# Performance work log

Measured on AMD Instinct MI355X. Metric: run time of the kernel, lower is better.

Reference implementation:

```python
import jax, jax.numpy as jnp
import numpy as np

LEAK = 0.9  # leaky-integrator rate of the ESN cell


def setup_inputs() -> dict:
    key = jax.random.key(0)
    ks = jax.random.split(key, 7)
    S, B, I, R = 512, 64, 256, 2048
    sc_in0 = 1.0 / np.sqrt(I)
    sc_h = 0.9 / np.sqrt(R)  # ~spectral-radius style scaling
    sc_in1 = 1.0 / np.sqrt(R)
    return {
        "x": jax.random.normal(ks[0], (S, B, I), jnp.float32),
        "W_in0": jax.random.normal(ks[1], (R, I), jnp.float32) * sc_in0,
        "W_hh0": jax.random.normal(ks[2], (R, R), jnp.float32) * sc_h,
        "b0": jax.random.normal(ks[3], (R,), jnp.float32) * 0.1,
        "W_in1": jax.random.normal(ks[4], (R, R), jnp.float32) * sc_in1,
        "W_hh1": jax.random.normal(ks[5], (R, R), jnp.float32) * sc_h,
        "b1": jax.random.normal(ks[6], (R,), jnp.float32) * 0.1,
    }


def _esn_layer(x_seq, W_in, W_hh, b):
    # x_seq: (S, B, D_in); returns (S, B, R), (B, R)
    B = x_seq.shape[1]
    R = W_hh.shape[0]
    h0 = jnp.zeros((B, R), x_seq.dtype)
    # Precompute input projection for all timesteps in one big GEMM.
    xin = jnp.einsum('sbd,rd->sbr', x_seq, W_in) + b

    def step(h, xin_t):
        h_new = (1.0 - LEAK) * h + LEAK * jnp.tanh(xin_t + h @ W_hh.T)
        return h_new, h_new

    h_n, ys = jax.lax.scan(step, h0, xin)
    return ys, h_n


def reference(x, W_in0, W_hh0, b0, W_in1, W_hh1, b1):
    y0, h0n = _esn_layer(x, W_in0, W_hh0, b0)
    y1, h1n = _esn_layer(y0, W_in1, W_hh1, b1)
    h_n = jnp.stack([h0n, h1n])  # (num_layers, B, R)
    return y1, h_n
```

## Files before the change

### kernel.cpp

```cpp
#include <hip/hip_runtime.h>

typedef _Float16 half8 __attribute__((ext_vector_type(8)));
typedef float floatx4 __attribute__((ext_vector_type(4)));

#define S_LEN 512
#define NB 64
#define NI 256
#define NR 2048
#define LEAK 0.9f

#define NBLK 128
#define TPB 512
#define LBLK 64
#define NBNR ((size_t)NB * NR)

#define OFF_BAR ((size_t)0)
#define OFF_H0  ((size_t)4096)
#define OFF_H1  (OFF_H0 + 2 * NBNR * 2)
#define OFF_XE  (OFF_H1 + 2 * NBNR * 2)

__device__ __forceinline__ half8 cvt8(const float* s) {
    float4 p = *(const float4*)s, q = *(const float4*)(s + 4);
    half8 v;
    v[0] = (_Float16)p.x; v[1] = (_Float16)p.y; v[2] = (_Float16)p.z; v[3] = (_Float16)p.w;
    v[4] = (_Float16)q.x; v[5] = (_Float16)q.y; v[6] = (_Float16)q.z; v[7] = (_Float16)q.w;
    return v;
}

__global__ void xprep_kernel(const float* __restrict__ x, _Float16* __restrict__ xe) {
    const int t = blockIdx.x;
    #pragma unroll
    for (int it = 0; it < 4; ++it) {
        const int u = it * 8 + (threadIdx.x >> 6);
        const int l = threadIdx.x & 63;
        const int b = (u >> 3) * 16 + (l & 15);
        const int i0 = (u & 7) * 32 + (l >> 4) * 8;
        half8 v = cvt8(x + ((size_t)t * NB + b) * NI + i0);
        *(half8*)(xe + (size_t)t * NB * NI + (size_t)u * 512 + (size_t)l * 8) = v;
    }
}

__device__ __forceinline__ void gbar(unsigned* bar) {
    __syncthreads();
    if (threadIdx.x == 0) {
        __threadfence();
        unsigned* cnt  = bar + (blockIdx.x & 7) * 32;
        unsigned* root = bar + 256;
        unsigned* gen  = bar + 272;
        unsigned g = __hip_atomic_load(gen, __ATOMIC_RELAXED, __HIP_MEMORY_SCOPE_AGENT);
        bool last = false;
        if (__hip_atomic_fetch_add(cnt, 1u, __ATOMIC_ACQ_REL, __HIP_MEMORY_SCOPE_AGENT) == (NBLK / 8 - 1)) {
            __hip_atomic_store(cnt, 0u, __ATOMIC_RELAXED, __HIP_MEMORY_SCOPE_AGENT);
            if (__hip_atomic_fetch_add(root, 1u, __ATOMIC_ACQ_REL, __HIP_MEMORY_SCOPE_AGENT) == 7u) {
                __hip_atomic_store(root, 0u, __ATOMIC_RELAXED, __HIP_MEMORY_SCOPE_AGENT);
                __hip_atomic_store(gen, g + 1u, __ATOMIC_RELEASE, __HIP_MEMORY_SCOPE_AGENT);
                last = true;
            }
        }
        if (!last)
            while (__hip_atomic_load(gen, __ATOMIC_RELAXED, __HIP_MEMORY_SCOPE_AGENT) == g)
                __builtin_amdgcn_s_sleep(1);
        __threadfence();
    }
    __syncthreads();
}

template <int CH, int KU, int ROLE>
__device__ __forceinline__ void esn_layer_run(
    const float* __restrict__ bias_v,
    const float* __restrict__ Whh, const float* __restrict__ Win,
    const char* __restrict__ xe,
    char* __restrict__ hp,
    const char* __restrict__ h0p,
    float* __restrict__ out,
    unsigned* __restrict__ bar,
    float* __restrict__ rsc, int r0)
{
    const int tid = threadIdx.x;
    const int l = tid & 63, w = tid >> 6, l15 = l & 15, g = l >> 4;

    half8 bwA[CH], bwB[CH];
    #pragma unroll
    for (int j = 0; j < CH; ++j) {
        const float* s0; int rs;
        if (j < 8) { s0 = Whh + (size_t)(r0 + l15) * NR + (w * 8 + j) * 32 + g * 8; rs = NR; }
        else if (ROLE == 0) { s0 = Win + (size_t)(r0 + l15) * KU + w * 32 + g * 8; rs = KU; }
        else { s0 = Win + (size_t)(r0 + l15) * KU + (w * 8 + j - 8) * 32 + g * 8; rs = KU; }
        bwA[j] = cvt8(s0);
        bwB[j] = cvt8(s0 + (size_t)16 * rs);
    }

    const int fg_o = w & 1, bt_o = w >> 1;
    const int ncol = r0 + fg_o * 16 + l15;
    const int bj0 = bt_o * 16 + g * 4;
    const float bias = bias_v[ncol];
    const int cu = ncol >> 5, gg = (ncol >> 3) & 3, ee = ncol & 7;
    float hs[4] = {0.f, 0.f, 0.f, 0.f};
    float* hn_base = out + (size_t)S_LEN * NBNR + (size_t)ROLE * NBNR;

    for (int s = 0; s < S_LEN + 1; ++s) {
        const int t = (ROLE == 0) ? s : s - 1;
        const bool active = (ROLE == 0) ? (s < S_LEN) : (s >= 1);
        if (active) {
            const char* hu = hp + (size_t)(t & 1) * (NBNR * 2);
            const char* uu = (ROLE == 0) ? xe + (size_t)t * NB * NI * 2
                                         : h0p + (size_t)((t + 1) & 1) * (NBNR * 2);

            floatx4 acc[2][4];
            #pragma unroll
            for (int fg = 0; fg < 2; ++fg)
                #pragma unroll
                for (int bt = 0; bt < 4; ++bt)
                    acc[fg][bt] = (floatx4){0.f, 0.f, 0.f, 0.f};

            #pragma unroll
            for (int bt = 0; bt < 4; ++bt) {
                half8 abuf[CH];
                #pragma unroll
                for (int j = 0; j < CH; ++j) {
                    const char* src; size_t unit;
                    if (j < 8)          { src = hu; unit = (size_t)(bt * 64 + w * 8 + j); }
                    else if (ROLE == 0) { src = uu; unit = (size_t)(bt * 8 + w); }
                    else                { src = uu; unit = (size_t)(bt * 64 + w * 8 + j - 8); }
                    abuf[j] = *(const half8*)(src + unit * 1024 + (size_t)l * 16);
                }
                #pragma unroll
                for (int j = 0; j < CH; ++j) {
                    acc[0][bt] = __builtin_amdgcn_mfma_f32_16x16x32_f16(abuf[j], bwA[j], acc[0][bt], 0, 0, 0);
                    acc[1][bt] = __builtin_amdgcn_mfma_f32_16x16x32_f16(abuf[j], bwB[j], acc[1][bt], 0, 0, 0);
                }
            }

            #pragma unroll
            for (int fg = 0; fg < 2; ++fg)
                #pragma unroll
                for (int bt = 0; bt < 4; ++bt)
                    *(floatx4*)(rsc + (size_t)((w * 8 + fg * 4 + bt) * 64 + l) * 4) = acc[fg][bt];
            __syncthreads();

            floatx4 r = {0.f, 0.f, 0.f, 0.f};
            #pragma unroll
            for (int v = 0; v < 8; ++v)
                r += *(const floatx4*)(rsc + (size_t)((v * 8 + fg_o * 4 + bt_o) * 64 + l) * 4);

            char* hw = hp + (size_t)((t + 1) & 1) * (NBNR * 2);
            #pragma unroll
            for (int j = 0; j < 4; ++j) {
                float hn = (1.0f - LEAK) * hs[j] + LEAK * tanhf(r[j] + bias);
                hs[j] = hn;
                const int bj = bj0 + j;
                size_t byte = (size_t)((bj >> 4) * 64 + cu) * 1024
                            + (size_t)((gg * 16 + (bj & 15)) * 8 + ee) * 2;
                *(_Float16*)(hw + byte) = (_Float16)hn;
                if (ROLE == 1)
                    __builtin_nontemporal_store(hn, out + (size_t)t * NBNR + (size_t)bj * NR + ncol);
                if (t == S_LEN - 1)
                    __builtin_nontemporal_store(hn, hn_base + (size_t)bj * NR + ncol);
            }
        }
        if (s < S_LEN) gbar(bar);
    }
}

__global__ void __launch_bounds__(TPB, 1) esn_kernel(
    const float* __restrict__ b0v, const float* __restrict__ b1v,
    const float* __restrict__ Whh0, const float* __restrict__ Win0,
    const float* __restrict__ Whh1, const float* __restrict__ Win1,
    const char* __restrict__ xe,
    char* __restrict__ h0p, char* __restrict__ h1p,
    unsigned* __restrict__ bar, float* __restrict__ out)
{
    __shared__ __align__(16) float rsc[64 * 64 * 4];
    const int bid = blockIdx.x;
    if (bid < LBLK)
        esn_layer_run<9, NI, 0>(b0v, Whh0, Win0, xe, h0p, nullptr,
                                out, bar, rsc, bid * 32);
    else
        esn_layer_run<16, NR, 1>(b1v, Whh1, Win1, nullptr, h1p, h0p,
                                 out, bar, rsc, (bid - LBLK) * 32);
}

extern "C" void kernel_launch(void* const* d_in, const int* in_sizes, int n_in,
                              void* d_out, int out_size, void* d_ws, size_t ws_size,
                              hipStream_t stream) {
    const float* x    = (const float*)d_in[0];
    const float* Win0 = (const float*)d_in[1];
    const float* Whh0 = (const float*)d_in[2];
    const float* b0   = (const float*)d_in[3];
    const float* Win1 = (const float*)d_in[4];
    const float* Whh1 = (const float*)d_in[5];
    const float* b1   = (const float*)d_in[6];

    char* ws = (char*)d_ws;
    char* xe  = ws + OFF_XE;
    char* h0p = ws + OFF_H0;
    char* h1p = ws + OFF_H1;
    unsigned* bar = (unsigned*)(ws + OFF_BAR);
    float* out = (float*)d_out;

    hipMemsetAsync(ws, 0, OFF_XE, stream);

    xprep_kernel<<<dim3(S_LEN), dim3(512), 0, stream>>>(x, (_Float16*)xe);

    void* args[] = { (void*)&b0, (void*)&b1, (void*)&Whh0, (void*)&Win0,
                     (void*)&Whh1, (void*)&Win1, (void*)&xe, (void*)&h0p,
                     (void*)&h1p, (void*)&bar, (void*)&out };
    hipError_t e = hipLaunchCooperativeKernel((void*)esn_kernel, dim3(NBLK), dim3(TPB),
                                              args, 0, stream);
    if (e != hipSuccess) {
        esn_kernel<<<dim3(NBLK), dim3(TPB), 0, stream>>>(
            b0, b1, Whh0, Win0, Whh1, Win1, xe, h0p, h1p, bar, out);
    }
}
```

Baseline: 8.902 ms.

## Split each ESN block's batch in half across 256 cooperative blocks with lighter barrier

```diff
diff --git a/kernel.cpp b/kernel.cpp
--- a/kernel.cpp
+++ b/kernel.cpp
@@ -9,9 +9,8 @@
 #define NR 2048
 #define LEAK 0.9f
 
-#define NBLK 128
+#define NBLK 256
 #define TPB 512
-#define LBLK 64
 #define NBNR ((size_t)NB * NR)
 
 #define OFF_BAR ((size_t)0)
@@ -40,16 +39,21 @@
     }
 }
 
+__device__ __forceinline__ void stH(_Float16* p, _Float16 v) {
+    unsigned short b;
+    __builtin_memcpy(&b, &v, 2);
+    __hip_atomic_store((unsigned short*)p, b, __ATOMIC_RELAXED, __HIP_MEMORY_SCOPE_AGENT);
+}
+
 __device__ __forceinline__ void gbar(unsigned* bar) {
     __syncthreads();
     if (threadIdx.x == 0) {
-        __threadfence();
         unsigned* cnt  = bar + (blockIdx.x & 7) * 32;
         unsigned* root = bar + 256;
         unsigned* gen  = bar + 272;
         unsigned g = __hip_atomic_load(gen, __ATOMIC_RELAXED, __HIP_MEMORY_SCOPE_AGENT);
         bool last = false;
-        if (__hip_atomic_fetch_add(cnt, 1u, __ATOMIC_ACQ_REL, __HIP_MEMORY_SCOPE_AGENT) == (NBLK / 8 - 1)) {
+        if (__hip_atomic_fetch_add(cnt, 1u, __ATOMIC_RELAXED, __HIP_MEMORY_SCOPE_AGENT) == (NBLK / 8 - 1)) {
             __hip_atomic_store(cnt, 0u, __ATOMIC_RELAXED, __HIP_MEMORY_SCOPE_AGENT);
             if (__hip_atomic_fetch_add(root, 1u, __ATOMIC_ACQ_REL, __HIP_MEMORY_SCOPE_AGENT) == 7u) {
                 __hip_atomic_store(root, 0u, __ATOMIC_RELAXED, __HIP_MEMORY_SCOPE_AGENT);
@@ -59,10 +63,10 @@
         }
         if (!last)
             while (__hip_atomic_load(gen, __ATOMIC_RELAXED, __HIP_MEMORY_SCOPE_AGENT) == g)
-                __builtin_amdgcn_s_sleep(1);
-        __threadfence();
+                __builtin_amdgcn_s_sleep(2);
     }
     __syncthreads();
+    __builtin_amdgcn_fence(__ATOMIC_ACQUIRE, "agent");
 }
 
 template <int CH, int KU, int ROLE>
@@ -74,7 +78,7 @@
     const char* __restrict__ h0p,
     float* __restrict__ out,
     unsigned* __restrict__ bar,
-    float* __restrict__ rsc, int r0)
+    float* __restrict__ rsc, int r0, int bhalf)
 {
     const int tid = threadIdx.x;
     const int l = tid & 63, w = tid >> 6, l15 = l & 15, g = l >> 4;
@@ -88,12 +92,14 @@
         else { s0 = Win + (size_t)(r0 + l15) * KU + (w * 8 + j - 8) * 32 + g * 8; rs = KU; }
         bwA[j] = cvt8(s0);
         bwB[j] = cvt8(s0 + (size_t)16 * rs);
-    }
-
-    const int fg_o = w & 1, bt_o = w >> 1;
+        asm volatile("" : "+v"(bwA[j]));
+        asm volatile("" : "+v"(bwB[j]));
+    }
+
+    const int fg_o = w & 1, bt_o = (w >> 1) & 1;
+    const bool owner = (w < 4);
     const int ncol = r0 + fg_o * 16 + l15;
-    const int bj0 = bt_o * 16 + g * 4;
-    const float bias = bias_v[ncol];
+    const float bias = owner ? bias_v[ncol] : 0.f;
     const int cu = ncol >> 5, gg = (ncol >> 3) & 3, ee = ncol & 7;
     float hs[4] = {0.f, 0.f, 0.f, 0.f};
     float* hn_base = out + (size_t)S_LEN * NBNR + (size_t)ROLE * NBNR;
@@ -106,22 +112,23 @@
             const char* uu = (ROLE == 0) ? xe + (size_t)t * NB * NI * 2
                                          : h0p + (size_t)((t + 1) & 1) * (NBNR * 2);
 
-            floatx4 acc[2][4];
+            floatx4 acc[2][2];
             #pragma unroll
             for (int fg = 0; fg < 2; ++fg)
                 #pragma unroll
-                for (int bt = 0; bt < 4; ++bt)
+                for (int bt = 0; bt < 2; ++bt)
                     acc[fg][bt] = (floatx4){0.f, 0.f, 0.f, 0.f};
 
             #pragma unroll
-            for (int bt = 0; bt < 4; ++bt) {
+            for (int bt = 0; bt < 2; ++bt) {
+                const int bt_g = bhalf * 2 + bt;
                 half8 abuf[CH];
                 #pragma unroll
                 for (int j = 0; j < CH; ++j) {
                     const char* src; size_t unit;
-                    if (j < 8)          { src = hu; unit = (size_t)(bt * 64 + w * 8 + j); }
-                    else if (ROLE == 0) { src = uu; unit = (size_t)(bt * 8 + w); }
-                    else                { src = uu; unit = (size_t)(bt * 64 + w * 8 + j - 8); }
+                    if (j < 8)          { src = hu; unit = (size_t)(bt_g * 64 + w * 8 + j); }
+                    else if (ROLE == 0) { src = uu; unit = (size_t)(bt_g * 8 + w); }
+                    else                { src = uu; unit = (size_t)(bt_g * 64 + w * 8 + j - 8); }
                     abuf[j] = *(const half8*)(src + unit * 1024 + (size_t)l * 16);
                 }
                 #pragma unroll
@@ -134,35 +141,37 @@
             #pragma unroll
             for (int fg = 0; fg < 2; ++fg)
                 #pragma unroll
-                for (int bt = 0; bt < 4; ++bt)
-                    *(floatx4*)(rsc + (size_t)((w * 8 + fg * 4 + bt) * 64 + l) * 4) = acc[fg][bt];
+                for (int bt = 0; bt < 2; ++bt)
+                    *(floatx4*)(rsc + (size_t)((w * 4 + bt * 2 + fg) * 64 + l) * 4) = acc[fg][bt];
             __syncthreads();
 
-            floatx4 r = {0.f, 0.f, 0.f, 0.f};
-            #pragma unroll
-            for (int v = 0; v < 8; ++v)
-                r += *(const floatx4*)(rsc + (size_t)((v * 8 + fg_o * 4 + bt_o) * 64 + l) * 4);
-
-            char* hw = hp + (size_t)((t + 1) & 1) * (NBNR * 2);
-            #pragma unroll
-            for (int j = 0; j < 4; ++j) {
-                float hn = (1.0f - LEAK) * hs[j] + LEAK * tanhf(r[j] + bias);
-                hs[j] = hn;
-                const int bj = bj0 + j;
-                size_t byte = (size_t)((bj >> 4) * 64 + cu) * 1024
-                            + (size_t)((gg * 16 + (bj & 15)) * 8 + ee) * 2;
-                *(_Float16*)(hw + byte) = (_Float16)hn;
-                if (ROLE == 1)
-                    __builtin_nontemporal_store(hn, out + (size_t)t * NBNR + (size_t)bj * NR + ncol);
-                if (t == S_LEN - 1)
-                    __builtin_nontemporal_store(hn, hn_base + (size_t)bj * NR + ncol);
+            if (owner) {
+                floatx4 r = {0.f, 0.f, 0.f, 0.f};
+                #pragma unroll
+                for (int v = 0; v < 8; ++v)
+                    r += *(const floatx4*)(rsc + (size_t)((v * 4 + w) * 64 + l) * 4);
+
+                char* hw = hp + (size_t)((t + 1) & 1) * (NBNR * 2);
+                #pragma unroll
+                for (int j = 0; j < 4; ++j) {
+                    float hn = (1.0f - LEAK) * hs[j] + LEAK * tanhf(r[j] + bias);
+                    hs[j] = hn;
+                    const int bj = bhalf * 32 + bt_o * 16 + g * 4 + j;
+                    size_t byte = (size_t)((bj >> 4) * 64 + cu) * 1024
+                                + (size_t)((gg * 16 + (bj & 15)) * 8 + ee) * 2;
+                    stH((_Float16*)(hw + byte), (_Float16)hn);
+                    if (ROLE == 1)
+                        __builtin_nontemporal_store(hn, out + (size_t)t * NBNR + (size_t)bj * NR + ncol);
+                    if (t == S_LEN - 1)
+                        __builtin_nontemporal_store(hn, hn_base + (size_t)bj * NR + ncol);
+                }
             }
         }
         if (s < S_LEN) gbar(bar);
     }
 }
 
-__global__ void __launch_bounds__(TPB, 1) esn_kernel(
+__global__ void __launch_bounds__(TPB, 2) esn_kernel(
     const float* __restrict__ b0v, const float* __restrict__ b1v,
     const float* __restrict__ Whh0, const float* __restrict__ Win0,
     const float* __restrict__ Whh1, const float* __restrict__ Win1,
@@ -170,14 +179,17 @@
     char* __restrict__ h0p, char* __restrict__ h1p,
     unsigned* __restrict__ bar, float* __restrict__ out)
 {
-    __shared__ __align__(16) float rsc[64 * 64 * 4];
+    __shared__ __align__(16) float rsc[32 * 64 * 4];
     const int bid = blockIdx.x;
-    if (bid < LBLK)
+    const int sub = bid & 127;
+    const int r0 = (sub >> 1) * 32;
+    const int bhalf = sub & 1;
+    if (bid < 128)
         esn_layer_run<9, NI, 0>(b0v, Whh0, Win0, xe, h0p, nullptr,
-                                out, bar, rsc, bid * 32);
+                                out, bar, rsc, r0, bhalf);
     else
         esn_layer_run<16, NR, 1>(b1v, Whh1, Win1, nullptr, h1p, h0p,
-                                 out, bar, rsc, (bid - LBLK) * 32);
+                                 out, bar, rsc, r0, bhalf);
 }
 
 extern "C" void kernel_launch(void* const* d_in, const int* in_sizes, int n_in,
@@ -198,7 +210,7 @@
     unsigned* bar = (unsigned*)(ws + OFF_BAR);
     float* out = (float*)d_out;
 
-    hipMemsetAsync(ws, 0, OFF_XE, stream);
+    (void)hipMemsetAsync(ws, 0, OFF_XE, stream);
 
     xprep_kernel<<<dim3(S_LEN), dim3(512), 0, stream>>>(x, (_Float16*)xe);
 
```

After: 10.98 ms. +23.3%, slower.

## Stream pre-converted fp16 weights each step instead of holding them in registers

Applied to the files above, without the earlier changes.

```diff
diff --git a/kernel.cpp b/kernel.cpp
--- a/kernel.cpp
+++ b/kernel.cpp
@@ -14,10 +14,19 @@
 #define LBLK 64
 #define NBNR ((size_t)NB * NR)
 
+#define CHT0 72
+#define CHT1 128
+
 #define OFF_BAR ((size_t)0)
 #define OFF_H0  ((size_t)4096)
 #define OFF_H1  (OFF_H0 + 2 * NBNR * 2)
 #define OFF_XE  (OFF_H1 + 2 * NBNR * 2)
+#define SZ_XE   ((size_t)S_LEN * NB * NI * 2)
+#define OFF_W0  (OFF_XE + SZ_XE)
+#define SZ_W0   ((size_t)128 * CHT0 * 1024)
+#define OFF_W1  (OFF_W0 + SZ_W0)
+#define SZ_W1   ((size_t)128 * CHT1 * 1024)
+#define WS_NEED (OFF_W1 + SZ_W1)
 
 __device__ __forceinline__ half8 cvt8(const float* s) {
     float4 p = *(const float4*)s, q = *(const float4*)(s + 4);
@@ -38,6 +47,22 @@
         half8 v = cvt8(x + ((size_t)t * NB + b) * NI + i0);
         *(half8*)(xe + (size_t)t * NB * NI + (size_t)u * 512 + (size_t)l * 8) = v;
     }
+}
+
+__global__ void wprep_kernel(const float* __restrict__ Whh0, const float* __restrict__ Win0,
+                             const float* __restrict__ Whh1, const float* __restrict__ Win1,
+                             _Float16* __restrict__ w0f, _Float16* __restrict__ w1f) {
+    int unit = blockIdx.x * 4 + (threadIdx.x >> 6);
+    const int l = threadIdx.x & 63;
+    const float* Whh; const float* Win; _Float16* dst; int CHT, KU;
+    if (unit < 128 * CHT0) { Whh = Whh0; Win = Win0; dst = w0f; CHT = CHT0; KU = NI; }
+    else { unit -= 128 * CHT0; Whh = Whh1; Win = Win1; dst = w1f; CHT = CHT1; KU = NR; }
+    const int fg = unit / CHT, ch = unit - fg * CHT;
+    const int feat = fg * 16 + (l & 15);
+    const int k = ch * 32 + (l >> 4) * 8;
+    const float* src = (k < NR) ? Whh + (size_t)feat * NR + k
+                                : Win + (size_t)feat * KU + (k - NR);
+    *(half8*)(dst + ((size_t)unit << 9) + (size_t)l * 8) = cvt8(src);
 }
 
 __device__ __forceinline__ void gbar(unsigned* bar) {
@@ -65,30 +90,27 @@
     __syncthreads();
 }
 
-template <int CH, int KU, int ROLE>
+__device__ __forceinline__ void stage8(half8* d, const char* src, int unitbase, int l) {
+    #pragma unroll
+    for (int jj = 0; jj < 8; ++jj)
+        d[jj] = *(const half8*)(src + ((size_t)(unitbase + jj) << 10) + (size_t)l * 16);
+}
+
+template <int ROLE, bool WF16>
 __device__ __forceinline__ void esn_layer_run(
     const float* __restrict__ bias_v,
-    const float* __restrict__ Whh, const float* __restrict__ Win,
+    const float* Whh, const float* Win,
+    const _Float16* __restrict__ wf,
     const char* __restrict__ xe,
-    char* __restrict__ hp,
-    const char* __restrict__ h0p,
+    char* hp, const char* h0p,
     float* __restrict__ out,
     unsigned* __restrict__ bar,
     float* __restrict__ rsc, int r0)
 {
     const int tid = threadIdx.x;
     const int l = tid & 63, w = tid >> 6, l15 = l & 15, g = l >> 4;
-
-    half8 bwA[CH], bwB[CH];
-    #pragma unroll
-    for (int j = 0; j < CH; ++j) {
-        const float* s0; int rs;
-        if (j < 8) { s0 = Whh + (size_t)(r0 + l15) * NR + (w * 8 + j) * 32 + g * 8; rs = NR; }
-        else if (ROLE == 0) { s0 = Win + (size_t)(r0 + l15) * KU + w * 32 + g * 8; rs = KU; }
-        else { s0 = Win + (size_t)(r0 + l15) * KU + (w * 8 + j - 8) * 32 + g * 8; rs = KU; }
-        bwA[j] = cvt8(s0);
-        bwB[j] = cvt8(s0 + (size_t)16 * rs);
-    }
+    constexpr int CHT = ROLE ? CHT1 : CHT0;
+    const int fg0 = r0 >> 4;
 
     const int fg_o = w & 1, bt_o = w >> 1;
     const int ncol = r0 + fg_o * 16 + l15;
@@ -113,21 +135,76 @@
                 for (int bt = 0; bt < 4; ++bt)
                     acc[fg][bt] = (floatx4){0.f, 0.f, 0.f, 0.f};
 
+            half8 wA[8], wB[8], ab[2][8];
+
+            if (WF16) {
+                const _Float16* p0 = wf + (((size_t)fg0 * CHT + w * 8) << 9) + (size_t)l * 8;
+                const _Float16* p1 = wf + (((size_t)(fg0 + 1) * CHT + w * 8) << 9) + (size_t)l * 8;
+                #pragma unroll
+                for (int jj = 0; jj < 8; ++jj) {
+                    wA[jj] = *(const half8*)(p0 + ((size_t)jj << 9));
+                    wB[jj] = *(const half8*)(p1 + ((size_t)jj << 9));
+                }
+            } else {
+                #pragma unroll
+                for (int jj = 0; jj < 8; ++jj) {
+                    wA[jj] = cvt8(Whh + (size_t)(r0 + l15) * NR + (w * 8 + jj) * 32 + g * 8);
+                    wB[jj] = cvt8(Whh + (size_t)(r0 + 16 + l15) * NR + (w * 8 + jj) * 32 + g * 8);
+                }
+            }
+            stage8(ab[0], hu, w * 8, l);
             #pragma unroll
             for (int bt = 0; bt < 4; ++bt) {
-                half8 abuf[CH];
-                #pragma unroll
-                for (int j = 0; j < CH; ++j) {
-                    const char* src; size_t unit;
-                    if (j < 8)          { src = hu; unit = (size_t)(bt * 64 + w * 8 + j); }
-                    else if (ROLE == 0) { src = uu; unit = (size_t)(bt * 8 + w); }
-                    else                { src = uu; unit = (size_t)(bt * 64 + w * 8 + j - 8); }
-                    abuf[j] = *(const half8*)(src + unit * 1024 + (size_t)l * 16);
-                }
-                #pragma unroll
-                for (int j = 0; j < CH; ++j) {
-                    acc[0][bt] = __builtin_amdgcn_mfma_f32_16x16x32_f16(abuf[j], bwA[j], acc[0][bt], 0, 0, 0);
-                    acc[1][bt] = __builtin_amdgcn_mfma_f32_16x16x32_f16(abuf[j], bwB[j], acc[1][bt], 0, 0, 0);
+                if (bt < 3) stage8(ab[(bt + 1) & 1], hu, (bt + 1) * 64 + w * 8, l);
+                #pragma unroll
+                for (int jj = 0; jj < 8; ++jj) {
+                    acc[0][bt] = __builtin_amdgcn_mfma_f32_16x16x32_f16(ab[bt & 1][jj], wA[jj], acc[0][bt], 0, 0, 0);
+                    acc[1][bt] = __builtin_amdgcn_mfma_f32_16x16x32_f16(ab[bt & 1][jj], wB[jj], acc[1][bt], 0, 0, 0);
+                }
+            }
+
+            if (ROLE == 1) {
+                if (WF16) {
+                    const _Float16* p0 = wf + (((size_t)fg0 * CHT + 64 + w * 8) << 9) + (size_t)l * 8;
+                    const _Float16* p1 = wf + (((size_t)(fg0 + 1) * CHT + 64 + w * 8) << 9) + (size_t)l * 8;
+                    #pragma unroll
+                    for (int jj = 0; jj < 8; ++jj) {
+                        wA[jj] = *(const half8*)(p0 + ((size_t)jj << 9));
+                        wB[jj] = *(const half8*)(p1 + ((size_t)jj << 9));
+                    }
+                } else {
+                    #pragma unroll
+                    for (int jj = 0; jj < 8; ++jj) {
+                        wA[jj] = cvt8(Win + (size_t)(r0 + l15) * NR + (w * 8 + jj) * 32 + g * 8);
+                        wB[jj] = cvt8(Win + (size_t)(r0 + 16 + l15) * NR + (w * 8 + jj) * 32 + g * 8);
+                    }
+                }
+                stage8(ab[0], uu, w * 8, l);
+                #pragma unroll
+                for (int bt = 0; bt < 4; ++bt) {
+                    if (bt < 3) stage8(ab[(bt + 1) & 1], uu, (bt + 1) * 64 + w * 8, l);
+                    #pragma unroll
+                    for (int jj = 0; jj < 8; ++jj) {
+                        acc[0][bt] = __builtin_amdgcn_mfma_f32_16x16x32_f16(ab[bt & 1][jj], wA[jj], acc[0][bt], 0, 0, 0);
+                        acc[1][bt] = __builtin_amdgcn_mfma_f32_16x16x32_f16(ab[bt & 1][jj], wB[jj], acc[1][bt], 0, 0, 0);
+                    }
+                }
+            } else {
+                half8 wiA, wiB, ai[4];
+                if (WF16) {
+                    wiA = *(const half8*)(wf + (((size_t)fg0 * CHT + 64 + w) << 9) + (size_t)l * 8);
+                    wiB = *(const half8*)(wf + (((size_t)(fg0 + 1) * CHT + 64 + w) << 9) + (size_t)l * 8);
+                } else {
+                    wiA = cvt8(Win + (size_t)(r0 + l15) * NI + w * 32 + g * 8);
+                    wiB = cvt8(Win + (size_t)(r0 + 16 + l15) * NI + w * 32 + g * 8);
+                }
+                #pragma unroll
+                for (int bt = 0; bt < 4; ++bt)
+                    ai[bt] = *(const half8*)(uu + ((size_t)(bt * 8 + w) << 10) + (size_t)l * 16);
+                #pragma unroll
+                for (int bt = 0; bt < 4; ++bt) {
+                    acc[0][bt] = __builtin_amdgcn_mfma_f32_16x16x32_f16(ai[bt], wiA, acc[0][bt], 0, 0, 0);
+                    acc[1][bt] = __builtin_amdgcn_mfma_f32_16x16x32_f16(ai[bt], wiB, acc[1][bt], 0, 0, 0);
                 }
             }
 
@@ -162,22 +239,24 @@
     }
 }
 
+template <bool WF16>
 __global__ void __launch_bounds__(TPB, 1) esn_kernel(
     const float* __restrict__ b0v, const float* __restrict__ b1v,
-    const float* __restrict__ Whh0, const float* __restrict__ Win0,
-    const float* __restrict__ Whh1, const float* __restrict__ Win1,
+    const float* Whh0, const float* Win0,
+    const float* Whh1, const float* Win1,
+    const _Float16* __restrict__ w0f, const _Float16* __restrict__ w1f,
     const char* __restrict__ xe,
-    char* __restrict__ h0p, char* __restrict__ h1p,
+    char* h0p, char* h1p,
     unsigned* __restrict__ bar, float* __restrict__ out)
 {
     __shared__ __align__(16) float rsc[64 * 64 * 4];
     const int bid = blockIdx.x;
     if (bid < LBLK)
-        esn_layer_run<9, NI, 0>(b0v, Whh0, Win0, xe, h0p, nullptr,
-                                out, bar, rsc, bid * 32);
+        esn_layer_run<0, WF16>(b0v, Whh0, Win0, w0f, xe, h0p, nullptr,
+                               out, bar, rsc, bid * 32);
     else
-        esn_layer_run<16, NR, 1>(b1v, Whh1, Win1, nullptr, h1p, h0p,
-                                 out, bar, rsc, (bid - LBLK) * 32);
+        esn_layer_run<1, WF16>(b1v, Whh1, Win1, w1f, nullptr, h1p, h0p,
+                               out, bar, rsc, (bid - LBLK) * 32);
 }
 
 extern "C" void kernel_launch(void* const* d_in, const int* in_sizes, int n_in,
@@ -196,19 +275,30 @@
     char* h0p = ws + OFF_H0;
     char* h1p = ws + OFF_H1;
     unsigned* bar = (unsigned*)(ws + OFF_BAR);
+    _Float16* w0f = (_Float16*)(ws + OFF_W0);
+    _Float16* w1f = (_Float16*)(ws + OFF_W1);
     float* out = (float*)d_out;
 
-    hipMemsetAsync(ws, 0, OFF_XE, stream);
-
+    const bool wf16 = (ws_size >= WS_NEED);
+
+    (void)hipMemsetAsync(ws, 0, OFF_XE, stream);
     xprep_kernel<<<dim3(S_LEN), dim3(512), 0, stream>>>(x, (_Float16*)xe);
+    if (wf16)
+        wprep_kernel<<<dim3((128 * (CHT0 + CHT1)) / 4), dim3(256), 0, stream>>>(
+            Whh0, Win0, Whh1, Win1, w0f, w1f);
 
     void* args[] = { (void*)&b0, (void*)&b1, (void*)&Whh0, (void*)&Win0,
-                     (void*)&Whh1, (void*)&Win1, (void*)&xe, (void*)&h0p,
-                     (void*)&h1p, (void*)&bar, (void*)&out };
-    hipError_t e = hipLaunchCooperativeKernel((void*)esn_kernel, dim3(NBLK), dim3(TPB),
+                     (void*)&Whh1, (void*)&Win1, (void*)&w0f, (void*)&w1f,
+                     (void*)&xe, (void*)&h0p, (void*)&h1p, (void*)&bar, (void*)&out };
+    void* fn = wf16 ? (void*)esn_kernel<true> : (void*)esn_kernel<false>;
+    hipError_t e = hipLaunchCooperativeKernel(fn, dim3(NBLK), dim3(TPB),
                                               args, 0, stream);
     if (e != hipSuccess) {
-        esn_kernel<<<dim3(NBLK), dim3(TPB), 0, stream>>>(
-            b0, b1, Whh0, Win0, Whh1, Win1, xe, h0p, h1p, bar, out);
+        if (wf16)
+            esn_kernel<true><<<dim3(NBLK), dim3(TPB), 0, stream>>>(
+                b0, b1, Whh0, Win0, Whh1, Win1, w0f, w1f, xe, h0p, h1p, bar, out);
+        else
+            esn_kernel<false><<<dim3(NBLK), dim3(TPB), 0, stream>>>(
+                b0, b1, Whh0, Win0, Whh1, Win1, w0f, w1f, xe, h0p, h1p, bar, out);
     }
 }
```

Result: slower. 9.593 ms (+7.8%).

## Double threads per block and split K reduction across 16 waves

Applied to the files above, without the earlier changes.

```diff
diff --git a/kernel.cpp b/kernel.cpp
--- a/kernel.cpp
+++ b/kernel.cpp
@@ -10,7 +10,7 @@
 #define LEAK 0.9f
 
 #define NBLK 128
-#define TPB 512
+#define TPB 1024
 #define LBLK 64
 #define NBNR ((size_t)NB * NR)
 
@@ -65,7 +65,7 @@
     __syncthreads();
 }
 
-template <int CH, int KU, int ROLE>
+template <int ROLE>
 __device__ __forceinline__ void esn_layer_run(
     const float* __restrict__ bias_v,
     const float* __restrict__ Whh, const float* __restrict__ Win,
@@ -78,22 +78,32 @@
 {
     const int tid = threadIdx.x;
     const int l = tid & 63, w = tid >> 6, l15 = l & 15, g = l >> 4;
-
-    half8 bwA[CH], bwB[CH];
+    constexpr int KU = ROLE ? NR : NI;
+
+    half8 wrA[4], wrB[4];
     #pragma unroll
-    for (int j = 0; j < CH; ++j) {
-        const float* s0; int rs;
-        if (j < 8) { s0 = Whh + (size_t)(r0 + l15) * NR + (w * 8 + j) * 32 + g * 8; rs = NR; }
-        else if (ROLE == 0) { s0 = Win + (size_t)(r0 + l15) * KU + w * 32 + g * 8; rs = KU; }
-        else { s0 = Win + (size_t)(r0 + l15) * KU + (w * 8 + j - 8) * 32 + g * 8; rs = KU; }
-        bwA[j] = cvt8(s0);
-        bwB[j] = cvt8(s0 + (size_t)16 * rs);
+    for (int j = 0; j < 4; ++j) {
+        const float* s = Whh + (size_t)(r0 + l15) * NR + (w * 4 + j) * 32 + g * 8;
+        wrA[j] = cvt8(s);
+        wrB[j] = cvt8(s + (size_t)16 * NR);
+    }
+    const int chi = (ROLE == 1) ? 4 : ((w >= 8) ? 1 : 0);
+    const int ci0 = (ROLE == 1) ? w * 4 : (w - 8);
+    half8 wiA[4], wiB[4];
+    #pragma unroll
+    for (int j = 0; j < 4; ++j) {
+        if (j < chi) {
+            const float* s = Win + (size_t)(r0 + l15) * KU + (ci0 + j) * 32 + g * 8;
+            wiA[j] = cvt8(s);
+            wiB[j] = cvt8(s + (size_t)16 * KU);
+        }
     }
 
     const int fg_o = w & 1, bt_o = w >> 1;
+    const bool owner = (w < 8);
     const int ncol = r0 + fg_o * 16 + l15;
     const int bj0 = bt_o * 16 + g * 4;
-    const float bias = bias_v[ncol];
+    const float bias = owner ? bias_v[ncol] : 0.f;
     const int cu = ncol >> 5, gg = (ncol >> 3) & 3, ee = ncol & 7;
     float hs[4] = {0.f, 0.f, 0.f, 0.f};
     float* hn_base = out + (size_t)S_LEN * NBNR + (size_t)ROLE * NBNR;
@@ -115,19 +125,30 @@
 
             #pragma unroll
             for (int bt = 0; bt < 4; ++bt) {
-                half8 abuf[CH];
-                #pragma unroll
-                for (int j = 0; j < CH; ++j) {
-                    const char* src; size_t unit;
-                    if (j < 8)          { src = hu; unit = (size_t)(bt * 64 + w * 8 + j); }
-                    else if (ROLE == 0) { src = uu; unit = (size_t)(bt * 8 + w); }
-                    else                { src = uu; unit = (size_t)(bt * 64 + w * 8 + j - 8); }
-                    abuf[j] = *(const half8*)(src + unit * 1024 + (size_t)l * 16);
-                }
-                #pragma unroll
-                for (int j = 0; j < CH; ++j) {
-                    acc[0][bt] = __builtin_amdgcn_mfma_f32_16x16x32_f16(abuf[j], bwA[j], acc[0][bt], 0, 0, 0);
-                    acc[1][bt] = __builtin_amdgcn_mfma_f32_16x16x32_f16(abuf[j], bwB[j], acc[1][bt], 0, 0, 0);
+                half8 ar[4];
+                #pragma unroll
+                for (int j = 0; j < 4; ++j)
+                    ar[j] = *(const half8*)(hu + ((size_t)(bt * 64 + w * 4 + j) << 10) + (size_t)l * 16);
+                #pragma unroll
+                for (int j = 0; j < 4; ++j) {
+                    acc[0][bt] = __builtin_amdgcn_mfma_f32_16x16x32_f16(ar[j], wrA[j], acc[0][bt], 0, 0, 0);
+                    acc[1][bt] = __builtin_amdgcn_mfma_f32_16x16x32_f16(ar[j], wrB[j], acc[1][bt], 0, 0, 0);
+                }
+                half8 av[4];
+                #pragma unroll
+                for (int j = 0; j < 4; ++j) {
+                    if (j < chi) {
+                        const size_t unit = (ROLE == 1) ? (size_t)(bt * 64 + ci0 + j)
+                                                        : (size_t)(bt * 8 + ci0);
+                        av[j] = *(const half8*)(uu + (unit << 10) + (size_t)l * 16);
+                    }
+                }
+                #pragma unroll
+                for (int j = 0; j < 4; ++j) {
+                    if (j < chi) {
+                        acc[0][bt] = __builtin_amdgcn_mfma_f32_16x16x32_f16(av[j], wiA[j], acc[0][bt], 0, 0, 0);
+                        acc[1][bt] = __builtin_amdgcn_mfma_f32_16x16x32_f16(av[j], wiB[j], acc[1][bt], 0, 0, 0);
+                    }
                 }
             }
 
@@ -138,24 +159,26 @@
                     *(floatx4*)(rsc + (size_t)((w * 8 + fg * 4 + bt) * 64 + l) * 4) = acc[fg][bt];
             __syncthreads();
 
-            floatx4 r = {0.f, 0.f, 0.f, 0.f};
-            #pragma unroll
-            for (int v = 0; v < 8; ++v)
-                r += *(const floatx4*)(rsc + (size_t)((v * 8 + fg_o * 4 + bt_o) * 64 + l) * 4);
-
-            char* hw = hp + (size_t)((t + 1) & 1) * (NBNR * 2);
-            #pragma unroll
-            for (int j = 0; j < 4; ++j) {
-                float hn = (1.0f - LEAK) * hs[j] + LEAK * tanhf(r[j] + bias);
-                hs[j] = hn;
-                const int bj = bj0 + j;
-                size_t byte = (size_t)((bj >> 4) * 64 + cu) * 1024
-                            + (size_t)((gg * 16 + (bj & 15)) * 8 + ee) * 2;
-                *(_Float16*)(hw + byte) = (_Float16)hn;
-                if (ROLE == 1)
-                    __builtin_nontemporal_store(hn, out + (size_t)t * NBNR + (size_t)bj * NR + ncol);
-                if (t == S_LEN - 1)
-                    __builtin_nontemporal_store(hn, hn_base + (size_t)bj * NR + ncol);
+            if (owner) {
+                floatx4 r = {0.f, 0.f, 0.f, 0.f};
+                #pragma unroll
+                for (int v = 0; v < 16; ++v)
+                    r += *(const floatx4*)(rsc + (size_t)((v * 8 + fg_o * 4 + bt_o) * 64 + l) * 4);
+
+                char* hw = hp + (size_t)((t + 1) & 1) * (NBNR * 2);
+                #pragma unroll
+                for (int j = 0; j < 4; ++j) {
+                    float hn = (1.0f - LEAK) * hs[j] + LEAK * tanhf(r[j] + bias);
+                    hs[j] = hn;
+                    const int bj = bj0 + j;
+                    size_t byte = (size_t)((bj >> 4) * 64 + cu) * 1024
+                                + (size_t)((gg * 16 + (bj & 15)) * 8 + ee) * 2;
+                    *(_Float16*)(hw + byte) = (_Float16)hn;
+                    if (ROLE == 1)
+                        __builtin_nontemporal_store(hn, out + (size_t)t * NBNR + (size_t)bj * NR + ncol);
+                    if (t == S_LEN - 1)
+                        __builtin_nontemporal_store(hn, hn_base + (size_t)bj * NR + ncol);
+                }
             }
         }
         if (s < S_LEN) gbar(bar);
@@ -170,14 +193,12 @@
     char* __restrict__ h0p, char* __restrict__ h1p,
     unsigned* __restrict__ bar, float* __restrict__ out)
 {
-    __shared__ __align__(16) float rsc[64 * 64 * 4];
+    __shared__ __align__(16) float rsc[128 * 64 * 4];
     const int bid = blockIdx.x;
     if (bid < LBLK)
-        esn_layer_run<9, NI, 0>(b0v, Whh0, Win0, xe, h0p, nullptr,
-                                out, bar, rsc, bid * 32);
+        esn_layer_run<0>(b0v, Whh0, Win0, xe, h0p, nullptr, out, bar, rsc, bid * 32);
     else
-        esn_layer_run<16, NR, 1>(b1v, Whh1, Win1, nullptr, h1p, h0p,
-                                 out, bar, rsc, (bid - LBLK) * 32);
+        esn_layer_run<1>(b1v, Whh1, Win1, nullptr, h1p, h0p, out, bar, rsc, (bid - LBLK) * 32);
 }
 
 extern "C" void kernel_launch(void* const* d_in, const int* in_sizes, int n_in,
@@ -198,7 +219,7 @@
     unsigned* bar = (unsigned*)(ws + OFF_BAR);
     float* out = (float*)d_out;
 
-    hipMemsetAsync(ws, 0, OFF_XE, stream);
+    (void)hipMemsetAsync(ws, 0, OFF_XE, stream);
 
     xprep_kernel<<<dim3(S_LEN), dim3(512), 0, stream>>>(x, (_Float16*)xe);
 
```

Measured after the change: 13.36 ms. 50.1% more time.
